# Kernel tuning notes

Hardware: AMD Instinct MI355X
Metric: run time of the kernel (lower is better)

## Reference

```python
import jax, jax.numpy as jnp
import numpy as np

N_NODES = 100000
N_EDGES = 800000
EMB = 256
NUM_LAYER = 5
BN_EPS = 1e-5


def setup_inputs() -> dict:
    key = jax.random.key(0)
    ks = jax.random.split(key, 16)
    s = 0.05
    return {
        "x_atom": jax.random.randint(ks[0], (N_NODES,), 0, 120, dtype=jnp.int32),
        "x_chir": jax.random.randint(ks[1], (N_NODES,), 0, 3, dtype=jnp.int32),
        "edge_src": jax.random.randint(ks[2], (N_EDGES,), 0, N_NODES, dtype=jnp.int32),
        "edge_dst": jax.random.randint(ks[3], (N_EDGES,), 0, N_NODES, dtype=jnp.int32),
        "ea_type": jax.random.randint(ks[4], (N_EDGES,), 0, 6, dtype=jnp.int32),
        "ea_dir": jax.random.randint(ks[5], (N_EDGES,), 0, 3, dtype=jnp.int32),
        "x_emb1": jax.random.normal(ks[6], (120, EMB), jnp.float32) * s,
        "x_emb2": jax.random.normal(ks[7], (3, EMB), jnp.float32) * s,
        "edge_emb1": jax.random.normal(ks[8], (NUM_LAYER, 6, EMB), jnp.float32) * s,
        "edge_emb2": jax.random.normal(ks[9], (NUM_LAYER, 3, EMB), jnp.float32) * s,
        "W1": jax.random.normal(ks[10], (NUM_LAYER, EMB, 2 * EMB), jnp.float32) * s,
        "b1": jnp.zeros((NUM_LAYER, 2 * EMB), jnp.float32),
        "W2": jax.random.normal(ks[11], (NUM_LAYER, 2 * EMB, EMB), jnp.float32) * s,
        "b2": jnp.zeros((NUM_LAYER, EMB), jnp.float32),
        "gamma": jnp.ones((NUM_LAYER, EMB), jnp.float32),
        "beta": jnp.zeros((NUM_LAYER, EMB), jnp.float32),
    }


def _gnn_forward(x_emb1, x_emb2, edge_emb1, edge_emb2, W1, b1, W2, b2, gamma, beta,
                 x_atom, x_chir, edge_src, edge_dst, ea_type, ea_dir):
    N = x_atom.shape[0]
    # node input embedding
    h = x_emb1[x_atom] + x_emb2[x_chir]  # [N, D]
    # add self loops (edge attr [4, 0] per original code)
    loop = jnp.arange(N, dtype=edge_src.dtype)
    src = jnp.concatenate([edge_src, loop])
    dst = jnp.concatenate([edge_dst, loop])
    et = jnp.concatenate([ea_type, jnp.full((N,), 4, dtype=ea_type.dtype)])
    ed = jnp.concatenate([ea_dir, jnp.zeros((N,), dtype=ea_dir.dtype)])
    L = W1.shape[0]
    for l in range(L):
        ee = edge_emb1[l][et] + edge_emb2[l][ed]          # [E+N, D]
        msg = h[src] + ee                                  # gather + edge embed
        agg = jax.ops.segment_sum(msg, dst, num_segments=N)  # scatter-add
        # 2-layer MLP update
        hl = jax.nn.relu(agg @ W1[l] + b1[l]) @ W2[l] + b2[l]
        # BatchNorm1d (training mode: biased batch statistics)
        mean = jnp.mean(hl, axis=0)
        var = jnp.mean(jnp.square(hl - mean), axis=0)
        hl = (hl - mean) * (gamma[l] / jnp.sqrt(var + BN_EPS)) + beta[l]
        # dropout with drop_ratio=0.0 is identity; relu on all but last layer
        if l < L - 1:
            hl = jax.nn.relu(hl)
        h = hl
    return h  # JK='last'


def reference(x_atom, x_chir, edge_src, edge_dst, ea_type, ea_dir,
              x_emb1, x_emb2, edge_emb1, edge_emb2, W1, b1, W2, b2, gamma, beta):
    return _gnn_forward(x_emb1, x_emb2, edge_emb1, edge_emb2, W1, b1, W2, b2,
                        gamma, beta, x_atom, x_chir, edge_src, edge_dst, ea_type, ea_dir)
```

## Files before the change

kernel.cpp:

```cpp
#include <hip/hip_runtime.h>
#include <cstdint>

typedef float f32x4 __attribute__((ext_vector_type(4)));
typedef __bf16 bf16x8 __attribute__((ext_vector_type(8)));
typedef unsigned short ushort4v __attribute__((ext_vector_type(4)));
typedef unsigned short u16;
typedef unsigned int u32;

__device__ __forceinline__ u16 f2bf(float f) {
  u32 u = __builtin_bit_cast(u32, f);
  u32 r = (u + 0x7fffu + ((u >> 16) & 1u)) >> 16;
  return (u16)r;
}

__device__ __forceinline__ float4 b2f4(ushort4v v) {
  float4 o;
  o.x = __builtin_bit_cast(float, (u32)v[0] << 16);
  o.y = __builtin_bit_cast(float, (u32)v[1] << 16);
  o.z = __builtin_bit_cast(float, (u32)v[2] << 16);
  o.w = __builtin_bit_cast(float, (u32)v[3] << 16);
  return o;
}

__device__ __forceinline__ void gload_lds16(const void* g, void* lds) {
  __builtin_amdgcn_global_load_lds(
      (const __attribute__((address_space(1))) u32*)g,
      (__attribute__((address_space(3))) u32*)lds,
      16, 0, 0);
}

__global__ __launch_bounds__(256) void k_cast_weights(
    const float* __restrict__ W1, const float* __restrict__ W2,
    u16* __restrict__ w1t, u16* __restrict__ w2t) {
  const int PER = 5 * 512 * 256;
  int idx = blockIdx.x * 256 + threadIdx.x;
  if (idx < PER) {
    int l = idx / (512 * 256);
    int rem = idx % (512 * 256);
    int n = rem / 256, k = rem % 256;
    w1t[idx] = f2bf(W1[l * 131072 + k * 512 + n]);
  } else if (idx < 2 * PER) {
    int j = idx - PER;
    int l = j / (256 * 512);
    int rem = j % (256 * 512);
    int n = rem / 512, k = rem % 512;
    w2t[j] = f2bf(W2[l * 131072 + k * 256 + n]);
  }
}

__global__ __launch_bounds__(256) void k_node_init(
    const int* __restrict__ xa, const int* __restrict__ xc,
    const float* __restrict__ e1, const float* __restrict__ e2,
    u16* __restrict__ h, int N) {
  int idx = blockIdx.x * 256 + threadIdx.x;
  if (idx >= N * 64) return;
  int node = idx >> 6, c = (idx & 63) * 4;
  int a = xa[node], ch = xc[node];
  float4 v1 = *(const float4*)&e1[a * 256 + c];
  float4 v2 = *(const float4*)&e2[ch * 256 + c];
  ushort4v o;
  o[0] = f2bf(v1.x + v2.x); o[1] = f2bf(v1.y + v2.y);
  o[2] = f2bf(v1.z + v2.z); o[3] = f2bf(v1.w + v2.w);
  *(ushort4v*)&h[(size_t)node * 256 + c] = o;
}

__global__ __launch_bounds__(256) void k_deg_count(
    const int* __restrict__ dst, int* __restrict__ deg, int E) {
  int e = blockIdx.x * 256 + threadIdx.x;
  if (e < E) atomicAdd(&deg[dst[e]], 1);
}

__global__ __launch_bounds__(256) void k_scan1(
    const int* __restrict__ deg, int* __restrict__ rp,
    int* __restrict__ bsum, int N) {
  __shared__ int s[256];
  int i = blockIdx.x * 256 + threadIdx.x;
  int v = (i < N) ? deg[i] : 0;
  s[threadIdx.x] = v;
  __syncthreads();
#pragma unroll
  for (int off = 1; off < 256; off <<= 1) {
    int t = (threadIdx.x >= off) ? s[threadIdx.x - off] : 0;
    __syncthreads();
    s[threadIdx.x] += t;
    __syncthreads();
  }
  if (i < N) rp[i] = s[threadIdx.x] - v;
  if (threadIdx.x == 255) bsum[blockIdx.x] = s[255];
}

__global__ __launch_bounds__(512) void k_scan2(
    const int* __restrict__ bsum, int* __restrict__ bexcl, int B) {
  __shared__ int s[512];
  int v = (threadIdx.x < B) ? bsum[threadIdx.x] : 0;
  s[threadIdx.x] = v;
  __syncthreads();
#pragma unroll
  for (int off = 1; off < 512; off <<= 1) {
    int t = (threadIdx.x >= off) ? s[threadIdx.x - off] : 0;
    __syncthreads();
    s[threadIdx.x] += t;
    __syncthreads();
  }
  if (threadIdx.x < B) bexcl[threadIdx.x] = s[threadIdx.x] - v;
}

__global__ __launch_bounds__(256) void k_scan3(
    int* __restrict__ rp, const int* __restrict__ bexcl,
    int* __restrict__ cur, int N, int E) {
  int i = blockIdx.x * 256 + threadIdx.x;
  if (i < N) {
    int v = rp[i] + bexcl[blockIdx.x];
    rp[i] = v;
    cur[i] = v;
  }
  if (i == 0) rp[N] = E;
}

__global__ __launch_bounds__(256) void k_fill(
    const int* __restrict__ src, const int* __restrict__ dst,
    const int* __restrict__ et, const int* __restrict__ ed,
    int* __restrict__ cur, u32* __restrict__ adj, int E) {
  int e = blockIdx.x * 256 + threadIdx.x;
  if (e >= E) return;
  int pos = atomicAdd(&cur[dst[e]], 1);
  adj[pos] = (u32)src[e] | ((u32)et[e] << 17) | ((u32)ed[e] << 20);
}

__global__ __launch_bounds__(256) void k_gather(
    const u16* __restrict__ h, const int* __restrict__ rp,
    const u32* __restrict__ adj, const float* __restrict__ ee1,
    const float* __restrict__ ee2, u16* __restrict__ aggb, int N) {
  int node = blockIdx.x * 4 + (threadIdx.x >> 6);
  if (node >= N) return;
  int lane = threadIdx.x & 63;
  int c = lane * 4;
  float4 a0 = b2f4(*(const ushort4v*)&h[(size_t)node * 256 + c]);
  float4 a1 = make_float4(0.f, 0.f, 0.f, 0.f);
  float4 a2 = a1, a3 = a1;
  u32 tcA = 0, tcB = 0;
  int beg = rp[node], end = rp[node + 1];
  int i = beg;
  for (; i + 4 <= end; i += 4) {
    u32 p0 = adj[i], p1 = adj[i + 1], p2 = adj[i + 2], p3 = adj[i + 3];
    float4 v0 = b2f4(*(const ushort4v*)&h[(size_t)(p0 & 0x1FFFF) * 256 + c]);
    float4 v1 = b2f4(*(const ushort4v*)&h[(size_t)(p1 & 0x1FFFF) * 256 + c]);
    float4 v2 = b2f4(*(const ushort4v*)&h[(size_t)(p2 & 0x1FFFF) * 256 + c]);
    float4 v3 = b2f4(*(const ushort4v*)&h[(size_t)(p3 & 0x1FFFF) * 256 + c]);
    a0.x += v0.x; a0.y += v0.y; a0.z += v0.z; a0.w += v0.w;
    a1.x += v1.x; a1.y += v1.y; a1.z += v1.z; a1.w += v1.w;
    a2.x += v2.x; a2.y += v2.y; a2.z += v2.z; a2.w += v2.w;
    a3.x += v3.x; a3.y += v3.y; a3.z += v3.z; a3.w += v3.w;
#pragma unroll
    for (int u = 0; u < 4; ++u) {
      u32 p = (u == 0) ? p0 : (u == 1) ? p1 : (u == 2) ? p2 : p3;
      u32 t = (p >> 17) & 7, r = (p >> 20) & 3;
      tcA += (t < 4) ? (1u << (t * 8)) : 0u;
      tcB += ((t == 4) ? 1u : 0u) + ((r == 0) ? 256u : 0u) +
             ((r == 1) ? 65536u : 0u);
    }
  }
  for (; i < end; ++i) {
    u32 p = adj[i];
    float4 v = b2f4(*(const ushort4v*)&h[(size_t)(p & 0x1FFFF) * 256 + c]);
    a0.x += v.x; a0.y += v.y; a0.z += v.z; a0.w += v.w;
    u32 t = (p >> 17) & 7, r = (p >> 20) & 3;
    tcA += (t < 4) ? (1u << (t * 8)) : 0u;
    tcB += ((t == 4) ? 1u : 0u) + ((r == 0) ? 256u : 0u) +
           ((r == 1) ? 65536u : 0u);
  }
  int deg = end - beg;
  int i0 = tcA & 255, i1 = (tcA >> 8) & 255, i2 = (tcA >> 16) & 255,
      i3 = (tcA >> 24) & 255;
  int i4 = (int)(tcB & 255) + 1;
  int r0 = (int)((tcB >> 8) & 255) + 1;
  int r1 = (int)((tcB >> 16) & 255);
  int i5 = deg - i0 - i1 - i2 - i3 - (i4 - 1);
  int r2 = deg - (r0 - 1) - r1;
  float ct[6], cr[3];
  ct[0] = (float)i0; ct[1] = (float)i1; ct[2] = (float)i2;
  ct[3] = (float)i3; ct[4] = (float)i4; ct[5] = (float)i5;
  cr[0] = (float)r0; cr[1] = (float)r1; cr[2] = (float)r2;

  float ax = a0.x + a1.x + a2.x + a3.x;
  float ay = a0.y + a1.y + a2.y + a3.y;
  float az = a0.z + a1.z + a2.z + a3.z;
  float aw = a0.w + a1.w + a2.w + a3.w;
#pragma unroll
  for (int t = 0; t < 6; ++t) {
    float4 e = *(const float4*)&ee1[t * 256 + c];
    ax += ct[t] * e.x; ay += ct[t] * e.y;
    az += ct[t] * e.z; aw += ct[t] * e.w;
  }
#pragma unroll
  for (int r = 0; r < 3; ++r) {
    float4 e = *(const float4*)&ee2[r * 256 + c];
    ax += cr[r] * e.x; ay += cr[r] * e.y;
    az += cr[r] * e.z; aw += cr[r] * e.w;
  }
  ushort4v o;
  o[0] = f2bf(ax); o[1] = f2bf(ay); o[2] = f2bf(az); o[3] = f2bf(aw);
  *(ushort4v*)&aggb[(size_t)node * 256 + c] = o;
}

template <int K, int NC, int OUTMODE, bool STATS>
__global__ __launch_bounds__(512) void k_gemm(
    const u16* __restrict__ A, const u16* __restrict__ Bt,
    const float* __restrict__ bias, void* __restrict__ outp,
    float* __restrict__ st, int M) {
  constexpr int NSTEP = K / 32;
  __shared__ u16 As[2][128 * 32];
  __shared__ u16 Bs[2][256 * 32];
  const int tid = threadIdx.x;
  const int lane = tid & 63;
  const int wv = tid >> 6;
  const int wrow = wv >> 2, wcol = wv & 3;
  const int m0 = blockIdx.x * 128;
  const int n0 = blockIdx.y * 256;
  const int fr = lane & 15;
  const int kgb = (lane >> 4) * 16;
  const int swz = (fr & 3) << 4;

  f32x4 acc[4][4];
#pragma unroll
  for (int m = 0; m < 4; ++m)
#pragma unroll
    for (int n = 0; n < 4; ++n) acc[m][n] = (f32x4){0.f, 0.f, 0.f, 0.f};

  auto stage = [&](int k0, int b) {
    {
      const int cidx = tid;
      int row = cidx >> 2, q = (cidx & 3) ^ (row & 3);
      int ar = m0 + row;
      if (ar >= M) ar = M - 1;
      gload_lds16(A + (size_t)ar * K + k0 + q * 8,
                  (char*)As[b] + (tid & ~63) * 16);
    }
#pragma unroll
    for (int j = 0; j < 2; ++j) {
      const int cidx = j * 512 + tid;
      int row = cidx >> 2, q = (cidx & 3) ^ (row & 3);
      gload_lds16(Bt + (size_t)(n0 + row) * K + k0 + q * 8,
                  (char*)Bs[b] + (j * 512 + (tid & ~63)) * 16);
    }
  };

  stage(0, 0);
  for (int ks = 0; ks < NSTEP; ++ks) {
    const int b = ks & 1;
    if (ks + 1 < NSTEP) {
      stage((ks + 1) * 32, b ^ 1);
      asm volatile("s_waitcnt vmcnt(3)" ::: "memory");
    } else {
      asm volatile("s_waitcnt vmcnt(0)" ::: "memory");
    }
    __builtin_amdgcn_sched_barrier(0);
    __builtin_amdgcn_s_barrier();
    __builtin_amdgcn_sched_barrier(0);
    bf16x8 af[4], bf[4];
#pragma unroll
    for (int m = 0; m < 4; ++m)
      af[m] = *(const bf16x8*)((const char*)As[b] +
                               (wrow * 64 + m * 16 + fr) * 64 + (kgb ^ swz));
#pragma unroll
    for (int n = 0; n < 4; ++n)
      bf[n] = *(const bf16x8*)((const char*)Bs[b] +
                               (wcol * 64 + n * 16 + fr) * 64 + (kgb ^ swz));
#pragma unroll
    for (int m = 0; m < 4; ++m)
#pragma unroll
      for (int n = 0; n < 4; ++n)
        acc[m][n] = __builtin_amdgcn_mfma_f32_16x16x32_bf16(af[m], bf[n],
                                                            acc[m][n], 0, 0, 0);
    __builtin_amdgcn_sched_barrier(0);
    __builtin_amdgcn_s_barrier();
  }

  float* sst = (float*)As;
  if (STATS) {
    __syncthreads();
    sst[tid] = 0.f;
    __syncthreads();
  }

  const int rb = (lane >> 4) * 4;
  float s[4], s2[4];
#pragma unroll
  for (int n = 0; n < 4; ++n) { s[n] = 0.f; s2[n] = 0.f; }
#pragma unroll
  for (int m = 0; m < 4; ++m) {
#pragma unroll
    for (int n = 0; n < 4; ++n) {
      const int col = n0 + wcol * 64 + n * 16 + fr;
      const float bv = bias[col];
#pragma unroll
      for (int j = 0; j < 4; ++j) {
        const int row = m0 + wrow * 64 + m * 16 + rb + j;
        if (row < M) {
          float v = acc[m][n][j] + bv;
          if (OUTMODE == 2) {
            v = fmaxf(v, 0.f);
            ((u16*)outp)[(size_t)row * NC + col] = f2bf(v);
          } else {
            ((float*)outp)[(size_t)row * NC + col] = v;
          }
          if (STATS) {
            s[n] += v;
            s2[n] += v * v;
          }
        }
      }
    }
  }
  if (STATS) {
#pragma unroll
    for (int n = 0; n < 4; ++n) {
      s[n] += __shfl_xor(s[n], 16);
      s[n] += __shfl_xor(s[n], 32);
      s2[n] += __shfl_xor(s2[n], 16);
      s2[n] += __shfl_xor(s2[n], 32);
    }
    if (lane < 16) {
#pragma unroll
      for (int n = 0; n < 4; ++n) {
        const int col = wcol * 64 + n * 16 + fr;
        atomicAdd(&sst[col], s[n]);
        atomicAdd(&sst[256 + col], s2[n]);
      }
    }
    __syncthreads();
    unsafeAtomicAdd(&st[tid], sst[tid]);
  }
}

__global__ __launch_bounds__(256) void k_bn_finalize(
    float* __restrict__ stats, const float* __restrict__ gamma,
    const float* __restrict__ beta, int l, float invN) {
  int c = threadIdx.x;
  float mean = stats[c] * invN;
  float var = stats[256 + c] * invN - mean * mean;
  float sc = gamma[l * 256 + c] * rsqrtf(var + 1e-5f);
  stats[512 + c] = sc;
  stats[768 + c] = beta[l * 256 + c] - mean * sc;
}

template <bool BF16RELU>
__global__ __launch_bounds__(256) void k_bn_apply(
    const float* __restrict__ hl, const float* __restrict__ stats,
    void* __restrict__ out, int N) {
  int idx = blockIdx.x * 256 + threadIdx.x;
  if (idx >= N * 64) return;
  int c = (idx & 63) * 4;
  float4 v = *(const float4*)&hl[(size_t)idx * 4];
  float4 sc = *(const float4*)&stats[512 + c];
  float4 sh = *(const float4*)&stats[768 + c];
  float4 o = make_float4(v.x * sc.x + sh.x, v.y * sc.y + sh.y,
                         v.z * sc.z + sh.z, v.w * sc.w + sh.w);
  if (BF16RELU) {
    ushort4v ob;
    ob[0] = f2bf(fmaxf(o.x, 0.f)); ob[1] = f2bf(fmaxf(o.y, 0.f));
    ob[2] = f2bf(fmaxf(o.z, 0.f)); ob[3] = f2bf(fmaxf(o.w, 0.f));
    *(ushort4v*)&((u16*)out)[(size_t)idx * 4] = ob;
  } else {
    *(float4*)&((float*)out)[(size_t)idx * 4] = o;
  }
}

extern "C" void kernel_launch(void* const* d_in, const int* in_sizes, int n_in,
                              void* d_out, int out_size, void* d_ws,
                              size_t ws_size, hipStream_t stream) {
  const int* x_atom = (const int*)d_in[0];
  const int* x_chir = (const int*)d_in[1];
  const int* esrc = (const int*)d_in[2];
  const int* edst = (const int*)d_in[3];
  const int* etype = (const int*)d_in[4];
  const int* edir = (const int*)d_in[5];
  const float* x_emb1 = (const float*)d_in[6];
  const float* x_emb2 = (const float*)d_in[7];
  const float* eemb1 = (const float*)d_in[8];
  const float* eemb2 = (const float*)d_in[9];
  const float* W1 = (const float*)d_in[10];
  const float* b1 = (const float*)d_in[11];
  const float* W2 = (const float*)d_in[12];
  const float* b2 = (const float*)d_in[13];
  const float* gamma = (const float*)d_in[14];
  const float* beta = (const float*)d_in[15];

  const int N = in_sizes[0];
  const int E = in_sizes[2];

  char* ws = (char*)d_ws;
  size_t off = 0;
  char* bufA = ws + off; off += (size_t)N * 1024;
  char* bufB = ws + off; off += (size_t)N * 1024;
  u16* aggb = (u16*)(ws + off); off += (size_t)N * 256 * 2;
  u16* w1t = (u16*)(ws + off); off += (size_t)5 * 512 * 256 * 2;
  u16* w2t = (u16*)(ws + off); off += (size_t)5 * 256 * 512 * 2;
  int* rp = (int*)(ws + off); off += (size_t)(N + 1) * 4;
  int* degcur = (int*)(ws + off); off += (size_t)N * 4;
  int* bsum = (int*)(ws + off); off += 512 * 4;
  int* bexcl = (int*)(ws + off); off += 512 * 4;
  u32* adj = (u32*)(ws + off); off += (size_t)E * 4;
  float* statsAll = (float*)(ws + off); off += 5 * 1024 * 4;

  const int gN64 = (N * 64 + 255) / 256;
  const int gE = (E + 255) / 256;
  const int B1 = (N + 255) / 256;
  const int NB128 = (N + 127) / 128;

  u16* hn = (u16*)bufA;
  u16* interb = (u16*)bufA;
  float* hl = (float*)bufB;

  hipMemsetAsync(degcur, 0, (size_t)N * 4, stream);
  hipMemsetAsync(statsAll, 0, 5 * 1024 * 4, stream);
  k_deg_count<<<gE, 256, 0, stream>>>(edst, degcur, E);
  k_scan1<<<B1, 256, 0, stream>>>(degcur, rp, bsum, N);
  k_scan2<<<1, 512, 0, stream>>>(bsum, bexcl, B1);
  k_scan3<<<B1, 256, 0, stream>>>(rp, bexcl, degcur, N, E);
  k_fill<<<gE, 256, 0, stream>>>(esrc, edst, etype, edir, degcur, adj, E);
  k_cast_weights<<<(2 * 5 * 512 * 256 + 255) / 256, 256, 0, stream>>>(W1, W2,
                                                                      w1t, w2t);
  k_node_init<<<gN64, 256, 0, stream>>>(x_atom, x_chir, x_emb1, x_emb2, hn, N);

  for (int l = 0; l < 5; ++l) {
    const float* ee1 = eemb1 + (size_t)l * 6 * 256;
    const float* ee2 = eemb2 + (size_t)l * 3 * 256;
    float* st = statsAll + l * 1024;

    k_gather<<<(N + 3) / 4, 256, 0, stream>>>(hn, rp, adj, ee1, ee2, aggb, N);
    k_gemm<256, 512, 2, false><<<dim3(NB128, 2), 512, 0, stream>>>(
        aggb, w1t + (size_t)l * 512 * 256, b1 + l * 512, interb, nullptr, N);
    k_gemm<512, 256, 0, true><<<dim3(NB128, 1), 512, 0, stream>>>(
        interb, w2t + (size_t)l * 256 * 512, b2 + l * 256, hl, st, N);
    k_bn_finalize<<<1, 256, 0, stream>>>(st, gamma, beta, l, 1.f / N);
    if (l < 4)
      k_bn_apply<true><<<gN64, 256, 0, stream>>>(hl, st, hn, N);
    else
      k_bn_apply<false><<<gN64, 256, 0, stream>>>(hl, st, d_out, N);
  }
}
```

Measured before the change: 1.416 ms.

## Add register-resident weight GEMM for first MLP layer and change LDS swizzle

Replaces the first MLP GEMM with a new kernel in which each wave keeps its 32-column slice of W1 in registers across all K and streams A rows straight from global memory, with no LDS staging or barriers. Each block processes 256 rows in 64-row chunks. It also changes the LDS XOR swizzle in the shared GEMM (used by the second layer) to a new pattern meant to cut bank conflicts. The risks are heavy register pressure from holding 16 bf16x8 weight fragments, uncoalesced per-lane A loads, and strided 2-byte output stores.

```diff
diff --git a/kernel.cpp b/kernel.cpp
--- a/kernel.cpp
+++ b/kernel.cpp
@@ -203,6 +203,70 @@
   *(ushort4v*)&aggb[(size_t)node * 256 + c] = o;
 }
 
+template <int K, int NC, int RPB>
+__global__ __launch_bounds__(256) void k_gemm1ws(
+    const u16* __restrict__ A, const u16* __restrict__ Bt,
+    const float* __restrict__ bias, u16* __restrict__ outp, int M) {
+  constexpr int KS = K / 32;
+  const int lane = threadIdx.x & 63;
+  const int w = threadIdx.x >> 6;
+  const int fr = lane & 15;
+  const int kg = lane >> 4;
+  const int rb = kg * 4;
+  const int n0 = blockIdx.y * 128 + w * 32;
+  const int mbase = blockIdx.x * RPB;
+
+  bf16x8 bq[2][KS];
+#pragma unroll
+  for (int h = 0; h < 2; ++h)
+#pragma unroll
+    for (int s = 0; s < KS; ++s)
+      bq[h][s] = *(const bf16x8*)&Bt[(size_t)(n0 + h * 16 + fr) * K +
+                                     s * 32 + kg * 8];
+  float bv[2];
+  bv[0] = bias[n0 + fr];
+  bv[1] = bias[n0 + 16 + fr];
+
+  for (int mc = 0; mc < RPB; mc += 64) {
+    const int m0 = mbase + mc;
+    if (m0 >= M) break;
+    f32x4 acc[4][2];
+#pragma unroll
+    for (int mf = 0; mf < 4; ++mf) {
+      acc[mf][0] = (f32x4){0.f, 0.f, 0.f, 0.f};
+      acc[mf][1] = (f32x4){0.f, 0.f, 0.f, 0.f};
+    }
+#pragma unroll
+    for (int mf = 0; mf < 4; ++mf) {
+      int row = m0 + mf * 16 + fr;
+      if (row >= M) row = M - 1;
+      bf16x8 af[KS];
+#pragma unroll
+      for (int s = 0; s < KS; ++s)
+        af[s] = *(const bf16x8*)&A[(size_t)row * K + s * 32 + kg * 8];
+#pragma unroll
+      for (int s = 0; s < KS; ++s) {
+        acc[mf][0] = __builtin_amdgcn_mfma_f32_16x16x32_bf16(af[s], bq[0][s],
+                                                             acc[mf][0], 0, 0, 0);
+        acc[mf][1] = __builtin_amdgcn_mfma_f32_16x16x32_bf16(af[s], bq[1][s],
+                                                             acc[mf][1], 0, 0, 0);
+      }
+    }
+#pragma unroll
+    for (int mf = 0; mf < 4; ++mf)
+#pragma unroll
+      for (int h = 0; h < 2; ++h)
+#pragma unroll
+        for (int j = 0; j < 4; ++j) {
+          int row = m0 + mf * 16 + rb + j;
+          if (row < M) {
+            float v = fmaxf(acc[mf][h][j] + bv[h], 0.f);
+            outp[(size_t)row * NC + n0 + h * 16 + fr] = f2bf(v);
+          }
+        }
+  }
+}
+
 template <int K, int NC, int OUTMODE, bool STATS>
 __global__ __launch_bounds__(512) void k_gemm(
     const u16* __restrict__ A, const u16* __restrict__ Bt,
@@ -218,8 +282,7 @@
   const int m0 = blockIdx.x * 128;
   const int n0 = blockIdx.y * 256;
   const int fr = lane & 15;
-  const int kgb = (lane >> 4) * 16;
-  const int swz = (fr & 3) << 4;
+  const int kg = lane >> 4;
 
   f32x4 acc[4][4];
 #pragma unroll
@@ -230,17 +293,19 @@
   auto stage = [&](int k0, int b) {
     {
       const int cidx = tid;
-      int row = cidx >> 2, q = (cidx & 3) ^ (row & 3);
+      const int lidx = cidx ^ ((cidx >> 3) & 7);
+      int row = lidx >> 2, kcol = lidx & 3;
       int ar = m0 + row;
       if (ar >= M) ar = M - 1;
-      gload_lds16(A + (size_t)ar * K + k0 + q * 8,
+      gload_lds16(A + (size_t)ar * K + k0 + kcol * 8,
                   (char*)As[b] + (tid & ~63) * 16);
     }
 #pragma unroll
     for (int j = 0; j < 2; ++j) {
       const int cidx = j * 512 + tid;
-      int row = cidx >> 2, q = (cidx & 3) ^ (row & 3);
-      gload_lds16(Bt + (size_t)(n0 + row) * K + k0 + q * 8,
+      const int lidx = cidx ^ ((cidx >> 3) & 7);
+      int row = lidx >> 2, kcol = lidx & 3;
+      gload_lds16(Bt + (size_t)(n0 + row) * K + k0 + kcol * 8,
                   (char*)Bs[b] + (j * 512 + (tid & ~63)) * 16);
     }
   };
@@ -259,13 +324,17 @@
     __builtin_amdgcn_sched_barrier(0);
     bf16x8 af[4], bf[4];
 #pragma unroll
-    for (int m = 0; m < 4; ++m)
-      af[m] = *(const bf16x8*)((const char*)As[b] +
-                               (wrow * 64 + m * 16 + fr) * 64 + (kgb ^ swz));
-#pragma unroll
-    for (int n = 0; n < 4; ++n)
-      bf[n] = *(const bf16x8*)((const char*)Bs[b] +
-                               (wcol * 64 + n * 16 + fr) * 64 + (kgb ^ swz));
+    for (int m = 0; m < 4; ++m) {
+      int row = wrow * 64 + m * 16 + fr;
+      int off = ((row << 2) + kg) ^ ((row >> 1) & 7);
+      af[m] = *(const bf16x8*)((const char*)As[b] + (off << 4));
+    }
+#pragma unroll
+    for (int n = 0; n < 4; ++n) {
+      int row = wcol * 64 + n * 16 + fr;
+      int off = ((row << 2) + kg) ^ ((row >> 1) & 7);
+      bf[n] = *(const bf16x8*)((const char*)Bs[b] + (off << 4));
+    }
 #pragma unroll
     for (int m = 0; m < 4; ++m)
 #pragma unroll
@@ -283,7 +352,7 @@
     __syncthreads();
   }
 
-  const int rb = (lane >> 4) * 4;
+  const int rb = kg * 4;
   float s[4], s2[4];
 #pragma unroll
   for (int n = 0; n < 4; ++n) { s[n] = 0.f; s2[n] = 0.f; }
@@ -407,6 +476,7 @@
   const int gE = (E + 255) / 256;
   const int B1 = (N + 255) / 256;
   const int NB128 = (N + 127) / 128;
+  const int GX = (N + 255) / 256;
 
   u16* hn = (u16*)bufA;
   u16* interb = (u16*)bufA;
@@ -429,8 +499,8 @@
     float* st = statsAll + l * 1024;
 
     k_gather<<<(N + 3) / 4, 256, 0, stream>>>(hn, rp, adj, ee1, ee2, aggb, N);
-    k_gemm<256, 512, 2, false><<<dim3(NB128, 2), 512, 0, stream>>>(
-        aggb, w1t + (size_t)l * 512 * 256, b1 + l * 512, interb, nullptr, N);
+    k_gemm1ws<256, 512, 256><<<dim3(GX, 4), 256, 0, stream>>>(
+        aggb, w1t + (size_t)l * 512 * 256, b1 + l * 512, interb, N);
     k_gemm<512, 256, 0, true><<<dim3(NB128, 1), 512, 0, stream>>>(
         interb, w2t + (size_t)l * 256 * 512, b2 + l * 256, hl, st, N);
     k_bn_finalize<<<1, 256, 0, stream>>>(st, gamma, beta, l, 1.f / N);
```

After: 1.620 ms. +14.4%, slower.
